# Kernel tuning notes

Hardware: AMD Instinct MI355X
Metric: run time of the kernel (lower is better)

## Reference

```python
import jax, jax.numpy as jnp
import numpy as np

B, N, F_IN, F_OUT, H = 8, 1024, 64, 128, 4
D = F_OUT // H  # head_dim = 32
NEG_SLOPE = 0.2


def setup_inputs() -> dict:
    key = jax.random.key(0)
    k1, k2, k3, k4, k5 = jax.random.split(key, 5)
    x = jax.random.normal(k1, (B, N, F_IN), dtype=jnp.float32)
    adj = jax.random.randint(k2, (N, N), 0, 2, dtype=jnp.int32)
    edge_weights = jax.random.uniform(k3, (N, N), dtype=jnp.float32)
    W = jax.random.normal(k4, (F_IN, F_OUT), dtype=jnp.float32) * (1.0 / np.sqrt(F_IN))
    a = jax.random.normal(k5, (H, 2 * D), dtype=jnp.float32) * (1.0 / np.sqrt(2 * D))
    return {"x": x, "adj": adj, "edge_weights": edge_weights, "W": W, "a": a}


def reference(x, adj, edge_weights, W, a):
    # x: [B,N,F_in], adj: [N,N] int, edge_weights: [N,N], W: [F_in,F_out], a: [H,2D]
    b, n, _ = x.shape
    h = (x @ W).reshape(b, n, H, D)  # [B,N,H,D]
    # e[b,i,j,h] = leaky_relu(a_src . h_i + a_dst . h_j)  (equivalent to concat trick)
    e_src = jnp.einsum('bnhd,hd->bnh', h, a[:, :D])  # [B,N,H]
    e_dst = jnp.einsum('bnhd,hd->bnh', h, a[:, D:])  # [B,N,H]
    e = jax.nn.leaky_relu(e_src[:, :, None, :] + e_dst[:, None, :, :], NEG_SLOPE)  # [B,N,N,H]
    mask = (adj == 0)[None, :, :, None]  # [1,N,N,1]
    e = jnp.where(mask, -jnp.inf, e)
    # numerically-stable softmax over neighbors (axis=2), matching torch reference
    e_max = jnp.max(e, axis=2, keepdims=True)
    e_max = jnp.where(jnp.isinf(e_max), 0.0, e_max)
    e_stable = e - e_max
    e_stable = jnp.where(jnp.isinf(e_stable), -100.0, e_stable)
    attn = jax.nn.softmax(e_stable, axis=2)
    attn = jnp.where(jnp.isnan(attn), 0.0, attn)
    # dropout is identity in eval mode
    attn = attn * edge_weights[None, :, :, None]  # [B,N,N,H]
    out = jnp.einsum('bijh,bjhd->bihd', attn, h).reshape(b, n, H * D)  # [B,N,F_out]
    avg_attn = attn.mean(axis=-1)  # [B,N,N]
    return out, avg_attn
```

## Files before the change

kernel.cpp:

```cpp
#include <hip/hip_runtime.h>
#include <hip/hip_fp16.h>

constexpr int B  = 8;
constexpr int N  = 1024;
constexpr int FI = 64;
constexpr int FO = 128;
constexpr int NH = 4;
constexpr float LOG2E = 1.4426950408889634f;

using half8 = __attribute__((ext_vector_type(8))) _Float16;
using f32x4 = __attribute__((ext_vector_type(4))) float;

union I8 { int4 v[2]; int s[8]; };
union F8 { float4 v[2]; float s[8]; };

__device__ __forceinline__ unsigned h2pack(float a, float b) {
  __half2 r = __float22half2_rn(make_float2(a, b));
  union { __half2 h; unsigned u; } c; c.h = r; return c.u;
}
__device__ __forceinline__ float h2f(unsigned short u) {
  union { unsigned short s; _Float16 h; } c; c.s = u; return (float)c.h;
}
__device__ __forceinline__ unsigned short f2h(float f) {
  __half hv = __float2half(f);
  return *reinterpret_cast<unsigned short*>(&hv);
}

__global__ __launch_bounds__(256, 2) void gat_prep(
    const float* __restrict__ x, const float* __restrict__ W,
    const float* __restrict__ a, const int* __restrict__ adj,
    const float* __restrict__ ew,
    unsigned short* __restrict__ h16,
    float* __restrict__ es, float* __restrict__ edt,
    unsigned short* __restrict__ mew) {
  const int t = threadIdx.x;
  if (blockIdx.x >= 512) {
    const size_t base = ((size_t)(blockIdx.x - 512) * 256 + t) * 8;
    I8 aj; aj.v[0] = *(const int4*)(adj + base); aj.v[1] = *(const int4*)(adj + base + 4);
    F8 e;  e.v[0]  = *(const float4*)(ew + base); e.v[1]  = *(const float4*)(ew + base + 4);
    union { unsigned short u[8]; uint4 v; } o;
    #pragma unroll
    for (int u = 0; u < 8; ++u)
      o.u[u] = aj.s[u] ? f2h(e.s[u]) : (unsigned short)0x8000;
    *(uint4*)(mew + base) = o.v;
    return;
  }
  __shared__ float xs[16 * FI];
  const int row0 = blockIdx.x * 16;
  for (int i = t; i < 16 * FI; i += 256) xs[i] = x[row0 * FI + i];
  const int f  = t & 127;
  const int rh = t >> 7;
  float wc[FI];
  #pragma unroll
  for (int k = 0; k < FI; ++k) wc[k] = W[k * FO + f];
  const int hh = f >> 5, d = f & 31;
  const float a_s = a[hh * 64 + d] * LOG2E;
  const float a_d = a[hh * 64 + 32 + d] * LOG2E;
  __syncthreads();
  float acc8[8];
  #pragma unroll
  for (int r = 0; r < 8; ++r) {
    const int lr = rh * 8 + r;
    const float4* xr = (const float4*)(xs + lr * FI);
    float acc = 0.f;
    #pragma unroll
    for (int kq = 0; kq < FI / 4; ++kq) {
      const float4 xv = xr[kq];
      acc += xv.x * wc[4*kq] + xv.y * wc[4*kq+1] + xv.z * wc[4*kq+2] + xv.w * wc[4*kq+3];
    }
    acc8[r] = acc;
    float ps = acc * a_s, pd = acc * a_d;
    #pragma unroll
    for (int off = 16; off; off >>= 1) {
      ps += __shfl_xor(ps, off, 64);
      pd += __shfl_xor(pd, off, 64);
    }
    const int row = row0 + lr;
    if (d == 0) {
      es[row * NH + hh] = ps;
      edt[((size_t)((row >> 10) * NH + hh)) * N + (row & 1023)] = pd;
    }
  }
  const int bb = row0 >> 10;
  const int jl = (row0 & 1023) + rh * 8;
  union { unsigned short u16[8]; uint4 v; } hv;
  #pragma unroll
  for (int r = 0; r < 8; ++r) hv.u16[r] = f2h(acc8[r]);
  const int ft = f >> 4, n = f & 15;
  const int sS = jl >> 5, kq2 = (jl >> 3) & 3;
  const size_t base = (size_t)bb * (FO * N)
                    + ((size_t)(ft * 32 + sS) * 64 + (n + 16 * kq2)) * 8;
  *(uint4*)(h16 + base) = hv.v;
}

__global__ __launch_bounds__(512, 4) void gat_attn(
    const unsigned short* __restrict__ h16,
    const float* __restrict__ es, const float* __restrict__ edt,
    const unsigned short* __restrict__ mew,
    float* __restrict__ out, float* __restrict__ avg) {
  __shared__ unsigned short pew[2][4 * 2048];
  __shared__ float edt_lds[NH * N];
  __shared__ float dvl[64];
  const int t  = threadIdx.x;
  const int b  = blockIdx.x & 7;
  const int i0 = (blockIdx.x >> 3) << 4;
  const int il = t >> 5, jq = t & 31;
  const int gi = i0 + il;
  float esv[4];
  { const float4 e4 = *(const float4*)(es + ((size_t)b * N + gi) * NH);
    esv[0] = e4.x; esv[1] = e4.y; esv[2] = e4.z; esv[3] = e4.w; }
  const int lane = t & 63, wave = t >> 6;
  const int hh = wave & 3, nt2 = wave >> 2;
  const int m = lane & 15, kq = lane >> 4;
  const int ft = hh * 2 + nt2;
  const unsigned short* hbp = h16 + (size_t)b * (FO * N) + (size_t)(ft * 32) * 512 + lane * 8;
  f32x4 acc0 = {0.f,0.f,0.f,0.f}, acc1 = {0.f,0.f,0.f,0.f};
  float dpart[4] = {0.f, 0.f, 0.f, 0.f};

  uint2  rmw;
  half8  Bf[4];

  auto ld_p1 = [&](int c) {
    const int jb = c * 128 + jq * 4;
    rmw = *(const uint2*)(mew + (size_t)gi * N + jb);
  };
  auto ld_B = [&](int c) {
    const size_t so = (size_t)c * 4 * 512;
    #pragma unroll
    for (int ks = 0; ks < 4; ++ks)
      Bf[ks] = *reinterpret_cast<const half8*>(hbp + so + (size_t)ks * 512);
  };
  auto p1_compute = [&](int c) {
    const int buf = c & 1;
    const int jb = c * 128 + jq * 4;
    union { uint2 v; unsigned short u[4]; } mw; mw.v = rmw;
    float4 red[4];
    #pragma unroll
    for (int h = 0; h < 4; ++h)
      red[h] = *(const float4*)(&edt_lds[h * N + jb]);
    const int g = jq >> 1, half = jq & 1;
    const int o = ((g * 16 + il) ^ (g & 7)) * 8 + half * 4;
    #pragma unroll
    for (int up = 0; up < 2; ++up) {
      float pk[4][2];
      #pragma unroll
      for (int uu = 0; uu < 2; ++uu) {
        const int u = up * 2 + uu;
        const float mfa = h2f((unsigned short)(mw.u[u] & 0x7fff));
        const float sgn = (mw.u[u] >> 15) ? 0.f : 1.f;
        #pragma unroll
        for (int h = 0; h < 4; ++h) {
          float e = esv[h] + (&red[h].x)[u];
          e = fmaxf(e, 0.2f * e);
          const float p = __builtin_amdgcn_exp2f(e);
          pk[h][uu] = p * mfa;
          dpart[h] = fmaf(p, sgn, dpart[h]);
        }
      }
      #pragma unroll
      for (int h = 0; h < 4; ++h)
        *(unsigned*)(pew[buf] + h * 2048 + o + up * 2) = h2pack(pk[h][0], pk[h][1]);
    }
  };
  auto p2_step = [&](int c) {
    const int buf = c & 1;
    #pragma unroll
    for (int ks = 0; ks < 4; ++ks) {
      const int g2 = ks * 4 + kq;
      const int o2 = ((g2 * 16 + m) ^ (g2 & 7)) * 8;
      half8 afr;
      { uint4 tmp = *(const uint4*)(pew[buf] + hh * 2048 + o2);
        __builtin_memcpy(&afr, &tmp, 16); }
      if (ks & 1)
        acc1 = __builtin_amdgcn_mfma_f32_16x16x32_f16(afr, Bf[ks], acc1, 0, 0, 0);
      else
        acc0 = __builtin_amdgcn_mfma_f32_16x16x32_f16(afr, Bf[ks], acc0, 0, 0, 0);
    }
  };

  { const float4* src = (const float4*)(edt + (size_t)b * NH * N);
    float4* dst = (float4*)edt_lds;
    dst[t]       = src[t];
    dst[t + 512] = src[t + 512]; }
  ld_B(0);
  ld_p1(0);
  __syncthreads();
  p1_compute(0);
  ld_p1(1);
  __syncthreads();

  #pragma unroll 1
  for (int c = 0; c < 8; ++c) {
    p2_step(c);
    if (c + 1 < 8) {
      ld_B(c + 1);
      p1_compute(c + 1);
      if (c + 2 < 8) ld_p1(c + 2);
      __syncthreads();
    }
  }

  #pragma unroll
  for (int h = 0; h < 4; ++h) {
    float v = dpart[h];
    v += __shfl_xor(v, 1, 64);  v += __shfl_xor(v, 2, 64);
    v += __shfl_xor(v, 4, 64);  v += __shfl_xor(v, 8, 64);
    v += __shfl_xor(v, 16, 64);
    if (jq == 0) dvl[il * NH + h] = v;
  }
  __syncthreads();
  if (t < 64) { const float dd = dvl[t]; dvl[t] = dd > 0.f ? 1.0f / dd : 0.f; }
  __syncthreads();
  #pragma unroll
  for (int reg = 0; reg < 4; ++reg) {
    const int row = kq * 4 + reg;
    const float inv = dvl[row * NH + hh];
    out[((size_t)b * N + i0 + row) * FO + hh * 32 + nt2 * 16 + m]
        = (acc0[reg] + acc1[reg]) * inv;
  }
  float inv4[4];
  #pragma unroll
  for (int h = 0; h < 4; ++h) inv4[h] = dvl[il * NH + h];
  #pragma unroll 1
  for (int c = 0; c < 8; ++c) {
    const int jb = c * 128 + jq * 4;
    union { uint2 v; unsigned short u[4]; } mw;
    mw.v = *(const uint2*)(mew + (size_t)gi * N + jb);
    float4 ed4[4];
    #pragma unroll
    for (int h = 0; h < 4; ++h)
      ed4[h] = *(const float4*)(&edt_lds[h * N + jb]);
    float4 r;
    float* rp = &r.x;
    #pragma unroll
    for (int u = 0; u < 4; ++u) {
      const float mfa = h2f((unsigned short)(mw.u[u] & 0x7fff));
      float sv = 0.f;
      #pragma unroll
      for (int h = 0; h < 4; ++h) {
        float e = esv[h] + (&ed4[h].x)[u];
        e = fmaxf(e, 0.2f * e);
        sv += __builtin_amdgcn_exp2f(e) * inv4[h];
      }
      rp[u] = 0.25f * mfa * sv;
    }
    *(float4*)(avg + ((size_t)b * N + gi) * N + jb) = r;
  }
}

extern "C" void kernel_launch(void* const* d_in, const int* in_sizes, int n_in,
                              void* d_out, int out_size, void* d_ws, size_t ws_size,
                              hipStream_t stream) {
  const float* x   = (const float*)d_in[0];
  const int*   adj = (const int*)d_in[1];
  const float* ewt = (const float*)d_in[2];
  const float* W   = (const float*)d_in[3];
  const float* a   = (const float*)d_in[4];

  float* out = (float*)d_out;
  float* avg = out + (size_t)B * N * FO;

  unsigned short* h16 = (unsigned short*)d_ws;
  unsigned short* mew = h16 + (size_t)B * FO * N;
  float* es   = (float*)(mew + (size_t)N * N);
  float* edt  = es + (size_t)B * N * NH;

  gat_prep<<<1024, 256, 0, stream>>>(x, W, a, adj, ewt, h16, es, edt, mew);
  gat_attn<<<B * (N / 16), 512, 0, stream>>>(h16, es, edt, mew, out, avg);
}
```

Baseline: 101.2 us.

## Precompute softmax denominators in a separate kernel and fuse avg_attn into main pass

Adds a gat_denom kernel that computes the per-row, per-head softmax denominator reciprocals ahead of time. The attention kernel reads them at entry, so it can write avg_attn directly inside the first pass instead of running a second sweep that recomputes exp over every row. This removes a duplicate exp pass and an extra global read of the mask/weight data, in exchange for one more kernel launch. That new kernel recomputes all exps once just for the denominators.

```diff
diff --git a/kernel.cpp b/kernel.cpp
--- a/kernel.cpp
+++ b/kernel.cpp
@@ -93,29 +93,80 @@
   *(uint4*)(h16 + base) = hv.v;
 }
 
+__global__ __launch_bounds__(256, 4) void gat_denom(
+    const float* __restrict__ es, const float* __restrict__ edt,
+    const unsigned short* __restrict__ mew,
+    float* __restrict__ dinv) {
+  const int blk = blockIdx.x;
+  const int b   = blk >> 8;
+  const int gi  = ((blk & 255) << 2) + (threadIdx.x >> 6);
+  const int lane = threadIdx.x & 63;
+  float esv[4];
+  { const float4 e4 = *(const float4*)(es + ((size_t)b * N + gi) * NH);
+    esv[0] = e4.x; esv[1] = e4.y; esv[2] = e4.z; esv[3] = e4.w; }
+  const int j0 = lane * 16;
+  union { uint2 v; unsigned short u[4]; } mw[4];
+  #pragma unroll
+  for (int q = 0; q < 4; ++q)
+    mw[q].v = *(const uint2*)(mew + (size_t)gi * N + j0 + q * 4);
+  float d[4] = {0.f, 0.f, 0.f, 0.f};
+  #pragma unroll
+  for (int h = 0; h < 4; ++h) {
+    const float* ep = edt + ((size_t)(b * NH + h)) * N + j0;
+    #pragma unroll
+    for (int q = 0; q < 4; ++q) {
+      const float4 ev = *(const float4*)(ep + q * 4);
+      #pragma unroll
+      for (int u = 0; u < 4; ++u) {
+        float e = esv[h] + (&ev.x)[u];
+        e = fmaxf(e, 0.2f * e);
+        const float sgn = (mw[q].u[u] >> 15) ? 0.f : 1.f;
+        d[h] = fmaf(__builtin_amdgcn_exp2f(e), sgn, d[h]);
+      }
+    }
+  }
+  #pragma unroll
+  for (int h = 0; h < 4; ++h) {
+    float v = d[h];
+    v += __shfl_xor(v, 1, 64);  v += __shfl_xor(v, 2, 64);
+    v += __shfl_xor(v, 4, 64);  v += __shfl_xor(v, 8, 64);
+    v += __shfl_xor(v, 16, 64); v += __shfl_xor(v, 32, 64);
+    d[h] = v;
+  }
+  if (lane == 0) {
+    float4 o;
+    o.x = d[0] > 0.f ? 1.0f / d[0] : 0.f;
+    o.y = d[1] > 0.f ? 1.0f / d[1] : 0.f;
+    o.z = d[2] > 0.f ? 1.0f / d[2] : 0.f;
+    o.w = d[3] > 0.f ? 1.0f / d[3] : 0.f;
+    *(float4*)(dinv + ((size_t)b * N + gi) * NH) = o;
+  }
+}
+
 __global__ __launch_bounds__(512, 4) void gat_attn(
     const unsigned short* __restrict__ h16,
     const float* __restrict__ es, const float* __restrict__ edt,
     const unsigned short* __restrict__ mew,
+    const float* __restrict__ dinv,
     float* __restrict__ out, float* __restrict__ avg) {
   __shared__ unsigned short pew[2][4 * 2048];
   __shared__ float edt_lds[NH * N];
-  __shared__ float dvl[64];
   const int t  = threadIdx.x;
   const int b  = blockIdx.x & 7;
   const int i0 = (blockIdx.x >> 3) << 4;
   const int il = t >> 5, jq = t & 31;
   const int gi = i0 + il;
-  float esv[4];
+  float esv[4], inv4[4];
   { const float4 e4 = *(const float4*)(es + ((size_t)b * N + gi) * NH);
     esv[0] = e4.x; esv[1] = e4.y; esv[2] = e4.z; esv[3] = e4.w; }
+  { const float4 v4 = *(const float4*)(dinv + ((size_t)b * N + gi) * NH);
+    inv4[0] = v4.x; inv4[1] = v4.y; inv4[2] = v4.z; inv4[3] = v4.w; }
   const int lane = t & 63, wave = t >> 6;
   const int hh = wave & 3, nt2 = wave >> 2;
   const int m = lane & 15, kq = lane >> 4;
   const int ft = hh * 2 + nt2;
   const unsigned short* hbp = h16 + (size_t)b * (FO * N) + (size_t)(ft * 32) * 512 + lane * 8;
   f32x4 acc0 = {0.f,0.f,0.f,0.f}, acc1 = {0.f,0.f,0.f,0.f};
-  float dpart[4] = {0.f, 0.f, 0.f, 0.f};
 
   uint2  rmw;
   half8  Bf[4];
@@ -140,6 +191,8 @@
       red[h] = *(const float4*)(&edt_lds[h * N + jb]);
     const int g = jq >> 1, half = jq & 1;
     const int o = ((g * 16 + il) ^ (g & 7)) * 8 + half * 4;
+    float4 r;
+    float* rp = &r.x;
     #pragma unroll
     for (int up = 0; up < 2; ++up) {
       float pk[4][2];
@@ -147,20 +200,22 @@
       for (int uu = 0; uu < 2; ++uu) {
         const int u = up * 2 + uu;
         const float mfa = h2f((unsigned short)(mw.u[u] & 0x7fff));
-        const float sgn = (mw.u[u] >> 15) ? 0.f : 1.f;
+        float sv = 0.f;
         #pragma unroll
         for (int h = 0; h < 4; ++h) {
           float e = esv[h] + (&red[h].x)[u];
           e = fmaxf(e, 0.2f * e);
           const float p = __builtin_amdgcn_exp2f(e);
           pk[h][uu] = p * mfa;
-          dpart[h] = fmaf(p, sgn, dpart[h]);
+          sv = fmaf(p, inv4[h], sv);
         }
+        rp[u] = 0.25f * mfa * sv;
       }
       #pragma unroll
       for (int h = 0; h < 4; ++h)
         *(unsigned*)(pew[buf] + h * 2048 + o + up * 2) = h2pack(pk[h][0], pk[h][1]);
     }
+    *(float4*)(avg + ((size_t)b * N + gi) * N + jb) = r;
   };
   auto p2_step = [&](int c) {
     const int buf = c & 1;
@@ -201,50 +256,11 @@
   }
 
   #pragma unroll
-  for (int h = 0; h < 4; ++h) {
-    float v = dpart[h];
-    v += __shfl_xor(v, 1, 64);  v += __shfl_xor(v, 2, 64);
-    v += __shfl_xor(v, 4, 64);  v += __shfl_xor(v, 8, 64);
-    v += __shfl_xor(v, 16, 64);
-    if (jq == 0) dvl[il * NH + h] = v;
-  }
-  __syncthreads();
-  if (t < 64) { const float dd = dvl[t]; dvl[t] = dd > 0.f ? 1.0f / dd : 0.f; }
-  __syncthreads();
-  #pragma unroll
   for (int reg = 0; reg < 4; ++reg) {
     const int row = kq * 4 + reg;
-    const float inv = dvl[row * NH + hh];
+    const float inv = dinv[((size_t)b * N + i0 + row) * NH + hh];
     out[((size_t)b * N + i0 + row) * FO + hh * 32 + nt2 * 16 + m]
         = (acc0[reg] + acc1[reg]) * inv;
-  }
-  float inv4[4];
-  #pragma unroll
-  for (int h = 0; h < 4; ++h) inv4[h] = dvl[il * NH + h];
-  #pragma unroll 1
-  for (int c = 0; c < 8; ++c) {
-    const int jb = c * 128 + jq * 4;
-    union { uint2 v; unsigned short u[4]; } mw;
-    mw.v = *(const uint2*)(mew + (size_t)gi * N + jb);
-    float4 ed4[4];
-    #pragma unroll
-    for (int h = 0; h < 4; ++h)
-      ed4[h] = *(const float4*)(&edt_lds[h * N + jb]);
-    float4 r;
-    float* rp = &r.x;
-    #pragma unroll
-    for (int u = 0; u < 4; ++u) {
-      const float mfa = h2f((unsigned short)(mw.u[u] & 0x7fff));
-      float sv = 0.f;
-      #pragma unroll
-      for (int h = 0; h < 4; ++h) {
-        float e = esv[h] + (&ed4[h].x)[u];
-        e = fmaxf(e, 0.2f * e);
-        sv += __builtin_amdgcn_exp2f(e) * inv4[h];
-      }
-      rp[u] = 0.25f * mfa * sv;
-    }
-    *(float4*)(avg + ((size_t)b * N + gi) * N + jb) = r;
   }
 }
 
@@ -264,7 +280,9 @@
   unsigned short* mew = h16 + (size_t)B * FO * N;
   float* es   = (float*)(mew + (size_t)N * N);
   float* edt  = es + (size_t)B * N * NH;
+  float* dinv = edt + (size_t)B * NH * N;
 
   gat_prep<<<1024, 256, 0, stream>>>(x, W, a, adj, ewt, h16, es, edt, mew);
-  gat_attn<<<B * (N / 16), 512, 0, stream>>>(h16, es, edt, mew, out, avg);
-}
+  gat_denom<<<B * (N / 4), 256, 0, stream>>>(es, edt, mew, dinv);
+  gat_attn<<<B * (N / 16), 512, 0, stream>>>(h16, es, edt, mew, dinv, out, avg);
+}
```

Measured after the change: 105.9 us. 4.6% more time.
